# Kernel tuning notes

Hardware: AMD Instinct MI355X
Metric: run time of the kernel (lower is better)

The kernel has to match this reference:

```python
import jax, jax.numpy as jnp
import numpy as np

N = 100000   # nodes
E = 1600000  # edges
NC = 10000   # candidates
G = 1000     # graphs
ND = 32      # node_emb_dim
ED = 8       # edge_emb_dim
L = 4        # num_layers


def setup_inputs() -> dict:
    key = jax.random.key(0)
    ks = jax.random.split(key, 12)
    s = 0.1
    return {
        "x": jax.random.normal(ks[0], (N, 2), dtype=jnp.float32),
        "edge_attr": jax.random.normal(ks[1], (E, 1), dtype=jnp.float32),
        "Wn_in": jax.random.normal(ks[2], (2, ND)) * s,
        "bn_in": jnp.zeros((ND,)),
        "We_in": jax.random.normal(ks[3], (1, ED)) * s,
        "be_in": jnp.zeros((ED,)),
        "We_l": jax.random.normal(ks[4], (L, 2 * ND + ED, ED)) * s,
        "be_l": jnp.zeros((L, ED)),
        "Wn_l": jax.random.normal(ks[5], (L, ND + ED, ND)) * s,
        "bn_l": jnp.zeros((L, ND)),
        "Wout": jax.random.normal(ks[6], (ND, 1)) * s,
        "bout": jnp.zeros((1,)),
        "edge_index": jax.random.randint(ks[7], (2, E), 0, N),
        "batch": jnp.sort(jax.random.randint(ks[8], (N,), 0, G)),
        "candidate_idxs": jax.random.randint(ks[9], (NC,), 0, N),
    }


def reference(x, edge_attr, Wn_in, bn_in, We_in, be_in, We_l, be_l, Wn_l, bn_l,
              Wout, bout, edge_index, batch, candidate_idxs):
    h = x @ Wn_in + bn_in            # [N, ND]
    e = edge_attr @ We_in + be_in    # [E, ED]
    src, dst = edge_index[0], edge_index[1]
    for l in range(L):
        # edge update: MLP on [x_src, x_dst, edge_attr]
        m = jnp.concatenate([h[src], h[dst], e], axis=-1)        # [E, 2*ND+ED]
        new_e = jax.nn.relu(m @ We_l[l] + be_l[l])               # [E, ED]
        # aggregate (aggr='add') messages at destination nodes
        agg = jax.ops.segment_sum(new_e, dst, num_segments=N)    # [N, ED]
        new_h = jax.nn.relu(jnp.concatenate([h, agg], axis=-1) @ Wn_l[l] + bn_l[l])
        h = h + new_h   # residual
        e = e + new_e   # residual
    logits = (h[candidate_idxs] @ Wout + bout)[:, 0]             # [NC]
    seg = batch[candidate_idxs]                                  # [NC] graph ids
    # scatter_log_softmax over per-graph candidate groups
    mx = jax.ops.segment_max(logits, seg, num_segments=G)
    shifted = logits - mx[seg]
    lse = jnp.log(jax.ops.segment_sum(jnp.exp(shifted), seg, num_segments=G))
    return shifted - lse[seg]
```

## Files before the change

### kernel.cpp

```cpp
#include <hip/hip_runtime.h>

#define ND 32
#define ED 8
#define NL 4
#define NG 1000
#define NBC_MAX 512
#define CHUNK 8192
#define CHUNK_H 4096

typedef unsigned short u16;


__device__ __forceinline__ u16 f2bf(float f) {
  unsigned u = __float_as_uint(f);
  u += 0x7fffu + ((u >> 16) & 1u);
  return (u16)(u >> 16);
}
__device__ __forceinline__ unsigned pack2(float a, float b) {
  return (unsigned)f2bf(a) | ((unsigned)f2bf(b) << 16);
}
__device__ __forceinline__ void cvt8(uint4 p, float* o) {
  o[0] = __uint_as_float(p.x << 16); o[1] = __uint_as_float(p.x & 0xffff0000u);
  o[2] = __uint_as_float(p.y << 16); o[3] = __uint_as_float(p.y & 0xffff0000u);
  o[4] = __uint_as_float(p.z << 16); o[5] = __uint_as_float(p.z & 0xffff0000u);
  o[6] = __uint_as_float(p.w << 16); o[7] = __uint_as_float(p.w & 0xffff0000u);
}
__device__ __forceinline__ uint4 pack8(const float* v) {
  uint4 o;
  o.x = pack2(v[0], v[1]); o.y = pack2(v[2], v[3]);
  o.z = pack2(v[4], v[5]); o.w = pack2(v[6], v[7]);
  return o;
}


__global__ void k_init_h(const float* __restrict__ x,
                         const float* __restrict__ W,
                         const float* __restrict__ b,
                         const float* __restrict__ We,
                         const float* __restrict__ be,
                         u16* __restrict__ h,
                         u16* __restrict__ zs, u16* __restrict__ zd,
                         int N) {
  int n = blockIdx.x * blockDim.x + threadIdx.x;
  if (n >= N) return;
  float x0 = x[2 * n], x1 = x[2 * n + 1];
  float v[ND];
#pragma unroll
  for (int d = 0; d < ND; ++d) v[d] = fmaf(x0, W[d], fmaf(x1, W[ND + d], b[d]));
#pragma unroll
  for (int d = 0; d < ND; ++d) v[d] = __uint_as_float((unsigned)f2bf(v[d]) << 16);
  uint4* h4 = reinterpret_cast<uint4*>(h + (size_t)n * ND);
#pragma unroll
  for (int q = 0; q < 4; ++q) h4[q] = pack8(&v[q * 8]);
  float zsv[ED], zdv[ED];
#pragma unroll
  for (int j = 0; j < ED; ++j) { zsv[j] = 0.0f; zdv[j] = be[j]; }
#pragma unroll
  for (int k = 0; k < ND; ++k)
#pragma unroll
    for (int j = 0; j < ED; ++j) {
      zsv[j] = fmaf(v[k], We[k * ED + j], zsv[j]);
      zdv[j] = fmaf(v[k], We[(ND + k) * ED + j], zdv[j]);
    }
  *reinterpret_cast<uint4*>(zs + (size_t)n * ED) = pack8(zsv);
  *reinterpret_cast<uint4*>(zd + (size_t)n * ED) = pack8(zdv);
}


__global__ void k_chist(const int* __restrict__ dst, int* __restrict__ bcnt,
                        int E, int nbc) {
  __shared__ int lcnt[NBC_MAX];
  for (int b = threadIdx.x; b < nbc; b += blockDim.x) lcnt[b] = 0;
  __syncthreads();
  int e0 = blockIdx.x * CHUNK_H;
  int e1 = min(e0 + CHUNK_H, E);
  for (int i = e0 + threadIdx.x; i < e1; i += blockDim.x)
    atomicAdd(&lcnt[dst[i] >> 8], 1);
  __syncthreads();
  for (int b = threadIdx.x; b < nbc; b += blockDim.x)
    if (lcnt[b]) atomicAdd(&bcnt[b], lcnt[b]);
}

__global__ void k_cscan(const int* __restrict__ bcnt, int* __restrict__ bbase,
                        int nbc) {
  __shared__ int s[NBC_MAX];
  int tid = threadIdx.x;
  if (nbc <= NBC_MAX) {
    int v = (tid < nbc) ? bcnt[tid] : 0;
    s[tid] = v;
    __syncthreads();
    for (int st = 1; st < NBC_MAX; st <<= 1) {
      int t = (tid >= st) ? s[tid - st] : 0;
      __syncthreads();
      s[tid] += t;
      __syncthreads();
    }
    if (tid < nbc) bbase[tid] = s[tid] - v;
    if (tid == nbc - 1) bbase[nbc] = s[tid];
  } else if (tid == 0) {
    int run = 0;
    for (int i = 0; i < nbc; ++i) { bbase[i] = run; run += bcnt[i]; }
    bbase[nbc] = run;
  }
}

__global__ void k_binA(const int* __restrict__ src, const int* __restrict__ dst,
                       const float* __restrict__ ea,
                       const int* __restrict__ bbase, int* __restrict__ cursor_c,
                       uint2* __restrict__ binned, int E, int nbc) {
  __shared__ int lcnt[NBC_MAX];
  __shared__ int lbase[NBC_MAX];
  for (int b = threadIdx.x; b < nbc; b += blockDim.x) lcnt[b] = 0;
  __syncthreads();
  int e0 = blockIdx.x * CHUNK;
  int e1 = min(e0 + CHUNK, E);
  for (int i = e0 + threadIdx.x; i < e1; i += blockDim.x)
    atomicAdd(&lcnt[dst[i] >> 8], 1);
  __syncthreads();
  for (int b = threadIdx.x; b < nbc; b += blockDim.x) {
    int c = lcnt[b];
    lbase[b] = c ? (bbase[b] + atomicAdd(&cursor_c[b], c)) : 0;
  }
  __syncthreads();
  for (int i = e0 + threadIdx.x; i < e1; i += blockDim.x) {
    int d = dst[i];
    int pos = atomicAdd(&lbase[d >> 8], 1);
    binned[pos] = make_uint2((unsigned)src[i] | ((unsigned)(d & 255) << 24),
                             __float_as_uint(ea[i]));
  }
}

__global__ void k_binB(const uint2* __restrict__ binned,
                       const int* __restrict__ bbase,
                       uint2* __restrict__ sedge, u16* __restrict__ e,
                       int* __restrict__ noffs,
                       const float* __restrict__ We,
                       const float* __restrict__ be,
                       int N) {
  __shared__ int hist[256];
  __shared__ int scn[256];
  int b = blockIdx.x;
  int base = bbase[b], end = bbase[b + 1];
  int node0 = b << 8;
  int nn = min(256, N - node0);
  hist[threadIdx.x] = 0;
  __syncthreads();
  for (int p = base + threadIdx.x; p < end; p += blockDim.x)
    atomicAdd(&hist[binned[p].x >> 24], 1);
  __syncthreads();
  int v = hist[threadIdx.x];
  scn[threadIdx.x] = v;
  __syncthreads();
  for (int st = 1; st < 256; st <<= 1) {
    int t = (threadIdx.x >= (unsigned)st) ? scn[threadIdx.x - st] : 0;
    __syncthreads();
    scn[threadIdx.x] += t;
    __syncthreads();
  }
  int excl = base + scn[threadIdx.x] - v;
  if ((int)threadIdx.x < nn) noffs[node0 + threadIdx.x] = excl;
  if (threadIdx.x == 0) noffs[min(node0 + 256, N)] = end;
  hist[threadIdx.x] = excl;
  __syncthreads();
  for (int p = base + threadIdx.x; p < end; p += blockDim.x) {
    uint2 rec = binned[p];
    int dl = (int)(rec.x >> 24);
    int pos = atomicAdd(&hist[dl], 1);
    sedge[pos] = make_uint2(rec.x & 0xffffffu, (unsigned)(node0 + dl));
    float a = __uint_as_float(rec.y);
    float e0[ED];
#pragma unroll
    for (int j = 0; j < ED; ++j) e0[j] = fmaf(a, We[j], be[j]);
    *reinterpret_cast<uint4*>(e + (size_t)pos * ED) = pack8(e0);
  }
}


template <bool LAST>
__global__ void k_edge(const u16* __restrict__ zs,
                       const u16* __restrict__ zd,
                       u16* __restrict__ e,
                       u16* __restrict__ ne,
                       const uint2* __restrict__ sedge,
                       const float* __restrict__ W3,
                       int E) {
  int nb = gridDim.x;
  int per = nb >> 3;
  int b = blockIdx.x;
  int lb = (b < (per << 3)) ? ((b & 7) * per + (b >> 3)) : b;
  int i = lb * blockDim.x + threadIdx.x;
  if (i >= E) return;
  uint2 sd = sedge[i];
  float zsv[ED], zdv[ED], ein[ED], acc[ED];
  cvt8(*reinterpret_cast<const uint4*>(zs + (size_t)sd.x * ED), zsv);
  cvt8(*reinterpret_cast<const uint4*>(zd + (size_t)sd.y * ED), zdv);
  cvt8(*reinterpret_cast<const uint4*>(e + (size_t)i * ED), ein);
#pragma unroll
  for (int j = 0; j < ED; ++j) acc[j] = zsv[j] + zdv[j];
#pragma unroll
  for (int k = 0; k < ED; ++k)
#pragma unroll
    for (int j = 0; j < ED; ++j)
      acc[j] = fmaf(ein[k], W3[k * ED + j], acc[j]);
#pragma unroll
  for (int j = 0; j < ED; ++j) acc[j] = fmaxf(acc[j], 0.0f);
  *reinterpret_cast<uint4*>(ne + (size_t)i * ED) = pack8(acc);
  if (!LAST) {
    float eo[ED];
#pragma unroll
    for (int j = 0; j < ED; ++j) eo[j] = ein[j] + acc[j];
    *reinterpret_cast<uint4*>(e + (size_t)i * ED) = pack8(eo);
  }
}

template <bool PROJ>
__global__ void k_node(u16* __restrict__ h,
                       const u16* __restrict__ ne,
                       const int* __restrict__ noffs,
                       const float* __restrict__ W,
                       const float* __restrict__ b,
                       const float* __restrict__ Wen,
                       const float* __restrict__ ben,
                       u16* __restrict__ zs, u16* __restrict__ zd,
                       int N) {
  int n = blockIdx.x * blockDim.x + threadIdx.x;
  if (n >= N) return;
  int o0 = noffs[n], o1 = noffs[n + 1];
  float av[ED];
#pragma unroll
  for (int j = 0; j < ED; ++j) av[j] = 0.0f;
  for (int p = o0; p < o1; ++p) {
    float t[ED];
    cvt8(*reinterpret_cast<const uint4*>(ne + (size_t)p * ED), t);
#pragma unroll
    for (int j = 0; j < ED; ++j) av[j] += t[j];
  }
  float acc[ND];
#pragma unroll
  for (int j = 0; j < ND; ++j) acc[j] = b[j];
  uint4* h4 = reinterpret_cast<uint4*>(h + (size_t)n * ND);
  float hv[ND];
#pragma unroll
  for (int q = 0; q < 4; ++q) cvt8(h4[q], &hv[q * 8]);
#pragma unroll
  for (int k = 0; k < ND; ++k)
#pragma unroll
    for (int j = 0; j < ND; ++j) acc[j] = fmaf(hv[k], W[k * ND + j], acc[j]);
#pragma unroll
  for (int k = 0; k < ED; ++k)
#pragma unroll
    for (int j = 0; j < ND; ++j) acc[j] = fmaf(av[k], W[(ND + k) * ND + j], acc[j]);
  float hn[ND];
#pragma unroll
  for (int k = 0; k < ND; ++k) {
    float o = hv[k] + fmaxf(acc[k], 0.0f);
    hn[k] = __uint_as_float((unsigned)f2bf(o) << 16);
  }
#pragma unroll
  for (int q = 0; q < 4; ++q) h4[q] = pack8(&hn[q * 8]);
  if (PROJ) {
    float zsv[ED], zdv[ED];
#pragma unroll
    for (int j = 0; j < ED; ++j) { zsv[j] = 0.0f; zdv[j] = ben[j]; }
#pragma unroll
    for (int k = 0; k < ND; ++k)
#pragma unroll
      for (int j = 0; j < ED; ++j) {
        zsv[j] = fmaf(hn[k], Wen[k * ED + j], zsv[j]);
        zdv[j] = fmaf(hn[k], Wen[(ND + k) * ED + j], zdv[j]);
      }
    *reinterpret_cast<uint4*>(zs + (size_t)n * ED) = pack8(zsv);
    *reinterpret_cast<uint4*>(zd + (size_t)n * ED) = pack8(zdv);
  }
}


__device__ __forceinline__ unsigned int enc_f32(float f) {
  unsigned int bits = __float_as_uint(f);
  return (bits & 0x80000000u) ? ~bits : (bits | 0x80000000u);
}
__device__ __forceinline__ float dec_f32(unsigned int u) {
  unsigned int bits = (u & 0x80000000u) ? (u ^ 0x80000000u) : ~u;
  return __uint_as_float(bits);
}

__global__ void k_logits(const u16* __restrict__ h,
                         const int* __restrict__ cand,
                         const int* __restrict__ batch,
                         const float* __restrict__ Wout,
                         const float* __restrict__ bout,
                         float* __restrict__ logits,
                         int* __restrict__ seg,
                         unsigned int* __restrict__ mxu,
                         int NC) {
  int c = blockIdx.x * blockDim.x + threadIdx.x;
  if (c >= NC) return;
  int idx = cand[c];
  const uint4* hr = reinterpret_cast<const uint4*>(h + (size_t)idx * ND);
  float acc = bout[0];
  float v[8];
#pragma unroll
  for (int q = 0; q < 4; ++q) {
    cvt8(hr[q], v);
#pragma unroll
    for (int k = 0; k < 8; ++k) acc = fmaf(v[k], Wout[q * 8 + k], acc);
  }
  logits[c] = acc;
  int g = batch[idx];
  seg[c] = g;
  atomicMax(&mxu[g], enc_f32(acc));
}

__global__ void k_expsum(float* __restrict__ logits,
                         const int* __restrict__ seg,
                         const unsigned int* __restrict__ mxu,
                         float* __restrict__ sum,
                         int NC) {
  int c = blockIdx.x * blockDim.x + threadIdx.x;
  if (c >= NC) return;
  int g = seg[c];
  float sh = logits[c] - dec_f32(mxu[g]);
  logits[c] = sh;
  atomicAdd(&sum[g], expf(sh));
}

__global__ void k_final(const float* __restrict__ shifted,
                        const int* __restrict__ seg,
                        const float* __restrict__ sum,
                        float* __restrict__ out, int NC) {
  int c = blockIdx.x * blockDim.x + threadIdx.x;
  if (c >= NC) return;
  out[c] = shifted[c] - logf(sum[seg[c]]);
}


extern "C" void kernel_launch(void* const* d_in, const int* in_sizes, int n_in,
                              void* d_out, int out_size, void* d_ws, size_t ws_size,
                              hipStream_t stream) {
  const float* x       = (const float*)d_in[0];
  const float* ea      = (const float*)d_in[1];
  const float* Wn_in   = (const float*)d_in[2];
  const float* bn_in   = (const float*)d_in[3];
  const float* We_in   = (const float*)d_in[4];
  const float* be_in   = (const float*)d_in[5];
  const float* We_l    = (const float*)d_in[6];
  const float* be_l    = (const float*)d_in[7];
  const float* Wn_l    = (const float*)d_in[8];
  const float* bn_l    = (const float*)d_in[9];
  const float* Wout    = (const float*)d_in[10];
  const float* bout    = (const float*)d_in[11];
  const int* edge_index= (const int*)d_in[12];
  const int* batch     = (const int*)d_in[13];
  const int* cand      = (const int*)d_in[14];

  const int N  = in_sizes[13];
  const int E  = in_sizes[1];
  const int NC = in_sizes[14];
  const int nbc = (N + 255) >> 8;

  char* ws = (char*)d_ws;
  uint2* binned = (uint2*)ws; ws += (size_t)E * sizeof(uint2);
  uint2* sedge  = (uint2*)ws; ws += (size_t)E * sizeof(uint2);
  u16*   h      = (u16*)ws;   ws += (size_t)N * ND * sizeof(u16);
  u16*   e      = (u16*)ws;   ws += (size_t)E * ED * sizeof(u16);
  u16*   ne     = (u16*)ws;   ws += (size_t)E * ED * sizeof(u16);
  u16*   zs     = (u16*)ws;   ws += (size_t)N * ED * sizeof(u16);
  u16*   zd     = (u16*)ws;   ws += (size_t)N * ED * sizeof(u16);
  int*   noffs  = (int*)ws;   ws += ((size_t)N + 4) * sizeof(int);
  int*   bcnt   = (int*)ws;   ws += (size_t)NBC_MAX * sizeof(int);
  int*   cursor = (int*)ws;   ws += (size_t)NBC_MAX * sizeof(int);
  int*   bbase  = (int*)ws;   ws += ((size_t)NBC_MAX + 4) * sizeof(int);
  float* logits = (float*)ws; ws += (size_t)NC * sizeof(float);
  int*   seg    = (int*)ws;   ws += (size_t)NC * sizeof(int);
  unsigned int* mxu = (unsigned int*)ws; ws += (size_t)NG * sizeof(unsigned int);
  float* sum    = (float*)ws; ws += (size_t)NG * sizeof(float);

  const int* srcp = edge_index;
  const int* dstp = edge_index + E;
  const int blk = 256;
  const size_t WE_STRIDE = (size_t)(2 * ND + ED) * ED;

  hipMemsetAsync(bcnt, 0, 2 * (size_t)NBC_MAX * sizeof(int), stream);
  k_chist<<<(E + CHUNK_H - 1) / CHUNK_H, 1024, 0, stream>>>(dstp, bcnt, E, nbc);
  k_cscan<<<1, NBC_MAX, 0, stream>>>(bcnt, bbase, nbc);
  k_binA<<<(E + CHUNK - 1) / CHUNK, 1024, 0, stream>>>(srcp, dstp, ea, bbase,
                                                       cursor, binned, E, nbc);
  k_binB<<<nbc, 256, 0, stream>>>(binned, bbase, sedge, e, noffs, We_in, be_in, N);

  k_init_h<<<(N + blk - 1) / blk, blk, 0, stream>>>(x, Wn_in, bn_in, We_l, be_l,
                                                    h, zs, zd, N);

  const int egrid = (E + blk - 1) / blk;
  const int ngrid = (N + blk - 1) / blk;
  for (int l = 0; l < NL; ++l) {
    const float* W3 = We_l + l * WE_STRIDE + (size_t)2 * ND * ED;
    const float* Wn = Wn_l + (size_t)l * (ND + ED) * ND;
    const float* bn = bn_l + (size_t)l * ND;
    if (l + 1 < NL) {
      k_edge<false><<<egrid, blk, 0, stream>>>(zs, zd, e, ne, sedge, W3, E);
      k_node<true><<<ngrid, blk, 0, stream>>>(
          h, ne, noffs, Wn, bn, We_l + (l + 1) * WE_STRIDE,
          be_l + (size_t)(l + 1) * ED, zs, zd, N);
    } else {
      k_edge<true><<<egrid, blk, 0, stream>>>(zs, zd, e, ne, sedge, W3, E);
      k_node<false><<<ngrid, blk, 0, stream>>>(
          h, ne, noffs, Wn, bn, nullptr, nullptr, nullptr, nullptr, N);
    }
  }

  hipMemsetAsync(mxu, 0, NG * (sizeof(unsigned int) + sizeof(float)), stream);
  k_logits<<<(NC + blk - 1) / blk, blk, 0, stream>>>(h, cand, batch, Wout, bout,
                                                     logits, seg, mxu, NC);
  k_expsum<<<(NC + blk - 1) / blk, blk, 0, stream>>>(logits, seg, mxu, sum, NC);
  k_final<<<(NC + blk - 1) / blk, blk, 0, stream>>>(logits, seg, sum,
                                                    (float*)d_out, NC);
}
```

Measured before the change: 359.6 us.

## Stage node incoming-edge messages in shared memory with coalesced cooperative loads

```diff
diff --git a/kernel.cpp b/kernel.cpp
--- a/kernel.cpp
+++ b/kernel.cpp
@@ -7,8 +7,15 @@
 #define NBC_MAX 512
 #define CHUNK 8192
 #define CHUNK_H 4096
+#define NPB 128
+#define NCH 1024
 
 typedef unsigned short u16;
+
+__device__ __forceinline__ int xcd_swizzle(int b, int nb) {
+  int per = nb >> 3;
+  return (b < (per << 3)) ? ((b & 7) * per + (b >> 3)) : b;
+}
 
 
 __device__ __forceinline__ u16 f2bf(float f) {
@@ -41,7 +48,7 @@
                          u16* __restrict__ h,
                          u16* __restrict__ zs, u16* __restrict__ zd,
                          int N) {
-  int n = blockIdx.x * blockDim.x + threadIdx.x;
+  int n = xcd_swizzle(blockIdx.x, gridDim.x) * blockDim.x + threadIdx.x;
   if (n >= N) return;
   float x0 = x[2 * n], x1 = x[2 * n + 1];
   float v[ND];
@@ -184,11 +191,7 @@
                        const uint2* __restrict__ sedge,
                        const float* __restrict__ W3,
                        int E) {
-  int nb = gridDim.x;
-  int per = nb >> 3;
-  int b = blockIdx.x;
-  int lb = (b < (per << 3)) ? ((b & 7) * per + (b >> 3)) : b;
-  int i = lb * blockDim.x + threadIdx.x;
+  int i = xcd_swizzle(blockIdx.x, gridDim.x) * blockDim.x + threadIdx.x;
   if (i >= E) return;
   uint2 sd = sedge[i];
   float zsv[ED], zdv[ED], ein[ED], acc[ED];
@@ -214,27 +217,43 @@
 }
 
 template <bool PROJ>
-__global__ void k_node(u16* __restrict__ h,
-                       const u16* __restrict__ ne,
-                       const int* __restrict__ noffs,
-                       const float* __restrict__ W,
-                       const float* __restrict__ b,
-                       const float* __restrict__ Wen,
-                       const float* __restrict__ ben,
-                       u16* __restrict__ zs, u16* __restrict__ zd,
-                       int N) {
-  int n = blockIdx.x * blockDim.x + threadIdx.x;
-  if (n >= N) return;
-  int o0 = noffs[n], o1 = noffs[n + 1];
+__global__ void __launch_bounds__(NPB)
+k_node(u16* __restrict__ h,
+       const u16* __restrict__ ne,
+       const int* __restrict__ noffs,
+       const float* __restrict__ W,
+       const float* __restrict__ b,
+       const float* __restrict__ Wen,
+       const float* __restrict__ ben,
+       u16* __restrict__ zs, u16* __restrict__ zd,
+       int N) {
+  __shared__ uint4 lne[NCH];
+  int lb = xcd_swizzle(blockIdx.x, gridDim.x);
+  int n0 = lb * NPB;
+  int n = n0 + threadIdx.x;
+  bool valid = n < N;
+  int base = noffs[n0];
+  int endall = noffs[min(n0 + NPB, N)];
+  int o0 = valid ? noffs[n] : base;
+  int o1 = valid ? noffs[n + 1] : base;
   float av[ED];
 #pragma unroll
   for (int j = 0; j < ED; ++j) av[j] = 0.0f;
-  for (int p = o0; p < o1; ++p) {
-    float t[ED];
-    cvt8(*reinterpret_cast<const uint4*>(ne + (size_t)p * ED), t);
-#pragma unroll
-    for (int j = 0; j < ED; ++j) av[j] += t[j];
-  }
+  for (int chunk = base; chunk < endall; chunk += NCH) {
+    int cnt = min(NCH, endall - chunk);
+    __syncthreads();
+    for (int t = threadIdx.x; t < cnt; t += NPB)
+      lne[t] = *reinterpret_cast<const uint4*>(ne + (size_t)(chunk + t) * ED);
+    __syncthreads();
+    int s = max(o0, chunk), epos = min(o1, chunk + cnt);
+    for (int p = s; p < epos; ++p) {
+      float t[ED];
+      cvt8(lne[p - chunk], t);
+#pragma unroll
+      for (int j = 0; j < ED; ++j) av[j] += t[j];
+    }
+  }
+  if (!valid) return;
   float acc[ND];
 #pragma unroll
   for (int j = 0; j < ND; ++j) acc[j] = b[j];
@@ -391,19 +410,19 @@
                                                     h, zs, zd, N);
 
   const int egrid = (E + blk - 1) / blk;
-  const int ngrid = (N + blk - 1) / blk;
+  const int ngrid = (N + NPB - 1) / NPB;
   for (int l = 0; l < NL; ++l) {
     const float* W3 = We_l + l * WE_STRIDE + (size_t)2 * ND * ED;
     const float* Wn = Wn_l + (size_t)l * (ND + ED) * ND;
     const float* bn = bn_l + (size_t)l * ND;
     if (l + 1 < NL) {
       k_edge<false><<<egrid, blk, 0, stream>>>(zs, zd, e, ne, sedge, W3, E);
-      k_node<true><<<ngrid, blk, 0, stream>>>(
+      k_node<true><<<ngrid, NPB, 0, stream>>>(
           h, ne, noffs, Wn, bn, We_l + (l + 1) * WE_STRIDE,
           be_l + (size_t)(l + 1) * ED, zs, zd, N);
     } else {
       k_edge<true><<<egrid, blk, 0, stream>>>(zs, zd, e, ne, sedge, W3, E);
-      k_node<false><<<ngrid, blk, 0, stream>>>(
+      k_node<false><<<ngrid, NPB, 0, stream>>>(
           h, ne, noffs, Wn, bn, nullptr, nullptr, nullptr, nullptr, N);
     }
   }
```

New measurement: 358.4 us. About the same (-0.3%).
